# Performance work log

Measured on AMD Instinct MI355X. Metric: run time of the kernel, lower is better.

## Reference

```python
import jax, jax.numpy as jnp
import numpy as np

# ---- static geometry derived from truncation (matches torch __init__) ----
T = 127
N_LAT_NH = T + 1                                   # 128 NH latitudes
LONS = [20 + 4 * i for i in range(N_LAT_NH)]       # octahedral reduced grid
CUMS = np.concatenate([[0], np.cumsum(np.array(LONS + LONS[::-1]))]).astype(int)
HZW_NH = np.minimum(4 + np.arange(N_LAT_NH), T)    # cubic truncation: m_max = nlon//4 - 1, capped at T
N_LATS_PER_M = np.array([(HZW_NH >= m).sum() for m in range(T + 1)])
L_SYM_FULL = (T + 3) // 2                          # 65 rows before dropping row 0
L_ANT = (T + 2) // 2                               # 64
N_VARS = 128
BATCH, ENS = 4, 1


def _tri_masks():
    """Zero-padded triangular structure of the per-m Legendre matrices."""
    sym = np.zeros((T + 1, L_SYM_FULL, N_LAT_NH), np.float32)
    ant = np.zeros((T + 1, L_ANT, N_LAT_NH), np.float32)
    for m in range(T + 1):
        n_lats = int(N_LATS_PER_M[m])
        ms = (T - m + 3) // 2
        off = L_SYM_FULL - ms
        sym[m, off:, N_LAT_NH - n_lats:] = 1.0
        if (m + 1) % 2 == 1:
            sym[m, off, :] = 0.0
        ma = (T - m + 2) // 2
        off = L_ANT - ma
        ant[m, off:, N_LAT_NH - n_lats:] = 1.0
        if m % 2 == 1:
            ant[m, off, :] = 0.0
    return sym[:, 1:, :], ant   # module drops first symmetric row -> [128,64,128]


def setup_inputs() -> dict:
    key = jax.random.key(0)
    k1, k2, k3 = jax.random.split(key, 3)
    n_grid = int(CUMS[-1])
    x = jax.random.normal(k1, (BATCH, ENS, n_grid, N_VARS), jnp.float32)
    sm, am = _tri_masks()
    # random stand-ins for (gaussian-weight-fused) Legendre polynomials, with the exact
    # triangular zero structure the module builds from ecTrans assets
    symmetric = jax.random.normal(k2, sm.shape, jnp.float32) * jnp.asarray(sm)
    antisymmetric = jax.random.normal(k3, am.shape, jnp.float32) * jnp.asarray(am)
    return {"x": x, "symmetric": symmetric, "antisymmetric": antisymmetric}


def reference(x, symmetric, antisymmetric):
    """Octahedral SHT forward: ragged longitudinal rfft -> hemispheric fold -> per-m Legendre matmuls.

    Returns spectrum [b, e, l, m, vars, 2] (real/imag stacked on last axis).
    """
    n_lat = 2 * N_LAT_NH
    north, south = [], []
    # loop is over structurally distinct (ragged) latitude ring lengths; NH lat i and its
    # SH mirror (lat n_lat-1-i) share nlon/truncation, so batch them in one FFT call.
    for i in range(N_LAT_NH):
        j = n_lat - 1 - i
        nlon = LONS[i]
        xn = x[:, :, CUMS[i]:CUMS[i + 1], :]           # [b,e,nlon,v]
        xs = x[:, :, CUMS[j]:CUMS[j + 1], :]
        xp = jnp.stack([xn, xs], axis=2)               # [b,e,2,nlon,v]
        f = jnp.fft.rfft(xp, axis=3) / nlon            # torch norm='forward'
        m_hi = int(HZW_NH[i]) + 1                      # keep m <= highest zonal wavenumber
        f = f[:, :, :, :m_hi, :]
        f = jnp.pad(f, ((0, 0), (0, 0), (0, 0), (0, T + 1 - m_hi), (0, 0)))
        north.append(f[:, :, 0])
        south.append(f[:, :, 1])                       # index i <-> lat n_lat-1-i: already pole-mirrored
    north = jnp.stack(north, axis=2)                   # [b,e,n_lat_nh,m,v] complex64
    south = jnp.stack(south, axis=2)
    # hemispheric symmetry of Legendre polynomials
    sym = north + south
    anti = north - south
    # per-m truncated Legendre contractions over NH latitudes (n)
    out_s = jnp.einsum('mln,benmv->belmv', symmetric, sym)     # [b,e,64,m,v]
    out_a = jnp.einsum('mln,benmv->belmv', antisymmetric, anti)
    # interleave symmetric (l-m even) and antisymmetric (l-m odd) rows -> full l axis (128)
    spec = jnp.stack([out_s, out_a], axis=3)
    b, e, L, _, M, V = spec.shape
    spec = spec.reshape(b, e, 2 * L, M, V)             # [b,e,l,m,v] complex, lower triangle zeros
    return jnp.stack([spec.real, spec.imag], axis=-1)  # real view [b,e,l,m,v,2]
```

## Files before the change

kernel.cpp:

```cpp
#include <hip/hip_runtime.h>
#include <math.h>

#define NGRID 70144
#define NV 128
#define JT 16
#define VS 64

__device__ __forceinline__ float4 f4add(float4 a, float4 b){ return make_float4(a.x+b.x, a.y+b.y, a.z+b.z, a.w+b.w); }
__device__ __forceinline__ float4 f4sub(float4 a, float4 b){ return make_float4(a.x-b.x, a.y-b.y, a.z-b.z, a.w-b.w); }

__device__ __forceinline__ long twoff_of(int i){
  long off = 0;
  for(int k=0;k<i;k++){
    int mh = (5+k < 128) ? (5+k) : 128;
    off += (long)mh * (long)(11 + 2*k);
  }
  return off;
}

__global__ void fill_tw(float* __restrict__ tw){
  int ring = blockIdx.x, mc = blockIdx.y;
  int N = 20 + 4*ring, H = N/2;
  int mhi = (5+ring < 128) ? (5+ring) : 128;
  int m0 = mc*32;
  if(m0 >= mhi) return;
  int m1 = (m0+32 < mhi) ? (m0+32) : mhi;
  long base = twoff_of(ring);
  int tot = (m1-m0)*(H+1);
  float invN = 1.0f / (float)N;
  for(int idx = threadIdx.x; idx < tot; idx += blockDim.x){
    int m = m0 + idx/(H+1);
    int j = idx % (H+1);
    int p = (m*j) % N;
    float th = 6.2831853071795864f * (float)p * invN;
    float sn, cs;
    __sincosf(th, &sn, &cs);
    long o = (base + (long)(m)*(H+1) + j)*2;
    tw[o]   = cs * invN;
    tw[o+1] = -sn * invN;
  }
}

__global__ __launch_bounds__(256) void dft_fold(const float* __restrict__ x,
                                                const float* __restrict__ tw,
                                                float* __restrict__ G){
  int ring = 127 - blockIdx.x;
  int mt = blockIdx.y;
  int b  = blockIdx.z >> 1;
  int vh = blockIdx.z & 1;
  int N = 20 + 4*ring, H = N/2, JC = H+1;
  int mhi = (5+ring < 128) ? (5+ring) : 128;
  int mbase = mt*32;
  if(mbase >= mhi) return;

  __shared__ __align__(16) float cS[JT][VS], sS[JT][VS], cA[JT][VS], sA[JT][VS];
  __shared__ __align__(16) float twl[JT][32][2];

  int tid = threadIdx.x;
  int vl = tid & 63;
  int mg = tid >> 6;
  int v  = vh*64 + vl;

  long twbase = twoff_of(ring);
  long offN = (long)ring*(2*ring+18);
  long a = ring+1;
  long offS = (long)NGRID - a*(2*a+18);
  const float* xn = x + ((long)b*NGRID + offN)*NV + vh*64;
  const float* xs = x + ((long)b*NGRID + offS)*NV + vh*64;

  float aSR[8], aSI[8], aAR[8], aAI[8];
  #pragma unroll
  for(int k=0;k<8;k++){ aSR[k]=0.f; aSI[k]=0.f; aAR[k]=0.f; aAI[k]=0.f; }

  int sjj = tid >> 4;
  int sv4 = (tid & 15) << 2;
  int tmp2 = (tid & 15) << 1;

  for(int j0=0; j0<JC; j0+=JT){
    __syncthreads();
    {
      int j = j0 + sjj;
      float4 z = make_float4(0.f,0.f,0.f,0.f);
      float4 nj=z, sj=z, np=z, sp=z;
      if(j < JC){
        nj = *(const float4*)&xn[(long)j*NV + sv4];
        sj = *(const float4*)&xs[(long)j*NV + sv4];
        if(j > 0 && j < H){
          int jp = N - j;
          np = *(const float4*)&xn[(long)jp*NV + sv4];
          sp = *(const float4*)&xs[(long)jp*NV + sv4];
        }
      }
      float4 e  = f4add(nj, sj);
      float4 o  = f4sub(nj, sj);
      float4 ep = f4add(np, sp);
      float4 op = f4sub(np, sp);
      *(float4*)&cS[sjj][sv4] = f4add(e, ep);
      *(float4*)&sS[sjj][sv4] = f4sub(e, ep);
      *(float4*)&cA[sjj][sv4] = f4add(o, op);
      *(float4*)&sA[sjj][sv4] = f4sub(o, op);
    }
    {
      int jsrc = j0 + sjj; if(jsrc > H) jsrc = H;
      int m0s = mbase + tmp2;     if(m0s > mhi-1) m0s = mhi-1;
      int m1s = mbase + tmp2 + 1; if(m1s > mhi-1) m1s = mhi-1;
      float2 t0 = *(const float2*)&tw[(twbase + (long)m0s*JC + jsrc)*2];
      float2 t1 = *(const float2*)&tw[(twbase + (long)m1s*JC + jsrc)*2];
      *(float4*)&twl[sjj][tmp2][0] = make_float4(t0.x, t0.y, t1.x, t1.y);
    }
    __syncthreads();
    int jlim = JC - j0; if(jlim > JT) jlim = JT;
    for(int jj=0; jj<jlim; jj++){
      float c_s = cS[jj][vl], s_s = sS[jj][vl], c_a = cA[jj][vl], s_a = sA[jj][vl];
      const float* twrow = &twl[jj][mg*8][0];
      #pragma unroll
      for(int k2=0; k2<4; k2++){
        float4 t4 = *(const float4*)&twrow[k2*4];
        aSR[2*k2]   += c_s*t4.x;  aSI[2*k2]   += s_s*t4.y;
        aAR[2*k2]   += c_a*t4.x;  aAI[2*k2]   += s_a*t4.y;
        aSR[2*k2+1] += c_s*t4.z;  aSI[2*k2+1] += s_s*t4.w;
        aAR[2*k2+1] += c_a*t4.z;  aAI[2*k2+1] += s_a*t4.w;
      }
    }
  }
  long gb = (long)ring*1024 + (long)b*256 + (long)v*2;
  #pragma unroll
  for(int k=0;k<8;k++){
    int m = mbase + mg*8 + k;
    if(m < mhi){
      long o = (long)m*131072 + gb;
      *(float2*)&G[o]             = make_float2(aSR[k], aSI[k]);
      *(float2*)&G[o + 16777216L] = make_float2(aAR[k], aAI[k]);
    }
  }
}

__global__ __launch_bounds__(256) void legendre_mm(const float* __restrict__ Wsym,
                                                   const float* __restrict__ Want,
                                                   const float* __restrict__ G,
                                                   float* __restrict__ out){
  int m = blockIdx.x, b = blockIdx.y, s = blockIdx.z;
  const float* W = s ? Want : Wsym;
  __shared__ __align__(16) float Wt[128][68];
  int tid = threadIdx.x;
  const float* Wm = W + (long)m*8192;
  for(int idx=tid; idx<8192; idx+=256){
    int l = idx >> 7, n = idx & 127;
    Wt[n][l] = Wm[idx];
  }
  __syncthreads();
  int v = tid & 127, lh = tid >> 7;
  int n0 = (m-4 > 0) ? (m-4) : 0;
  const float* Gs = G + (long)s*16777216 + (long)m*131072 + (long)b*256 + (long)v*2;
  float aR[32], aI[32];
  #pragma unroll
  for(int q=0;q<32;q++){ aR[q]=0.f; aI[q]=0.f; }
  #pragma unroll 2
  for(int n=n0; n<128; n++){
    float2 g = *(const float2*)&Gs[(long)n*1024];
    const float* wrow = &Wt[n][lh*32];
    #pragma unroll
    for(int q2=0; q2<8; q2++){
      float4 w = *(const float4*)&wrow[q2*4];
      aR[q2*4+0] += w.x*g.x; aI[q2*4+0] += w.x*g.y;
      aR[q2*4+1] += w.y*g.x; aI[q2*4+1] += w.y*g.y;
      aR[q2*4+2] += w.z*g.x; aI[q2*4+2] += w.z*g.y;
      aR[q2*4+3] += w.w*g.x; aI[q2*4+3] += w.w*g.y;
    }
  }
  #pragma unroll
  for(int q=0;q<32;q++){
    int l = lh*32 + q;
    int lf = 2*l + s;
    long o = (((long)b*128 + lf)*128 + m)*256 + (long)v*2;
    *(float2*)&out[o] = make_float2(aR[q], aI[q]);
  }
}

extern "C" void kernel_launch(void* const* d_in, const int* in_sizes, int n_in,
                              void* d_out, int out_size, void* d_ws, size_t ws_size,
                              hipStream_t stream) {
  const float* x    = (const float*)d_in[0];
  const float* Wsym = (const float*)d_in[1];
  const float* Want = (const float*)d_in[2];
  float* out = (float*)d_out;
  float* ws  = (float*)d_ws;

  long two = 0;
  for(int k=0;k<128;k++){ int mh = (5+k<128)?(5+k):128; two += (long)mh*(long)(11+2*k); }
  long GBASE = (two*2 + 255) & ~255L;

  float* tw = ws;
  float* G  = ws + GBASE;

  hipLaunchKernelGGL(fill_tw,     dim3(128,4),   dim3(256), 0, stream, tw);
  hipLaunchKernelGGL(dft_fold,    dim3(128,4,8), dim3(256), 0, stream, x, tw, G);
  hipLaunchKernelGGL(legendre_mm, dim3(128,4,2), dim3(256), 0, stream, Wsym, Want, G, out);
}
```

Measured before the change: 428.8 us.

## Move Legendre contraction to bf16 MFMA with hi/lo split for precision

The FP32 FMA Legendre matmul is replaced by an MFMA kernel that uses bf16x3 emulation (hi*hi + lo*hi + hi*lo). The DFT stage now writes its output split into bf16 high and low parts. A new kernel splits the Legendre weights into bf16 hi/lo parts, reusing the twiddle workspace after the DFT stage has finished with it. The B tile is staged in swizzled shared memory, and all-zero K blocks are skipped for large m. This should cut ALU time in the matmul stage, at the cost of an extra launch and a small loss of accuracy from the dropped lo*lo term.

```diff
diff --git a/kernel.cpp b/kernel.cpp
--- a/kernel.cpp
+++ b/kernel.cpp
@@ -6,8 +6,17 @@
 #define JT 16
 #define VS 64
 
+typedef float f32x4 __attribute__((ext_vector_type(4)));
+typedef short short8 __attribute__((ext_vector_type(8)));
+
 __device__ __forceinline__ float4 f4add(float4 a, float4 b){ return make_float4(a.x+b.x, a.y+b.y, a.z+b.z, a.w+b.w); }
 __device__ __forceinline__ float4 f4sub(float4 a, float4 b){ return make_float4(a.x-b.x, a.y-b.y, a.z-b.z, a.w-b.w); }
+
+__device__ __forceinline__ unsigned f2bf(float f){
+  unsigned u = __float_as_uint(f);
+  return (u + 0x7FFFu + ((u>>16)&1u)) >> 16;
+}
+__device__ __forceinline__ float bf2f(unsigned h){ return __uint_as_float(h<<16); }
 
 __device__ __forceinline__ long twoff_of(int i){
   long off = 0;
@@ -43,7 +52,8 @@
 
 __global__ __launch_bounds__(256) void dft_fold(const float* __restrict__ x,
                                                 const float* __restrict__ tw,
-                                                float* __restrict__ G){
+                                                unsigned short* __restrict__ Gh,
+                                                unsigned short* __restrict__ Gl){
   int ring = 127 - blockIdx.x;
   int mt = blockIdx.y;
   int b  = blockIdx.z >> 1;
@@ -129,51 +139,102 @@
     int m = mbase + mg*8 + k;
     if(m < mhi){
       long o = (long)m*131072 + gb;
-      *(float2*)&G[o]             = make_float2(aSR[k], aSI[k]);
-      *(float2*)&G[o + 16777216L] = make_float2(aAR[k], aAI[k]);
-    }
-  }
-}
-
-__global__ __launch_bounds__(256) void legendre_mm(const float* __restrict__ Wsym,
-                                                   const float* __restrict__ Want,
-                                                   const float* __restrict__ G,
-                                                   float* __restrict__ out){
+      unsigned h0 = f2bf(aSR[k]), h1 = f2bf(aSI[k]);
+      unsigned l0 = f2bf(aSR[k] - bf2f(h0)), l1 = f2bf(aSI[k] - bf2f(h1));
+      *(unsigned*)&Gh[o] = h0 | (h1<<16);
+      *(unsigned*)&Gl[o] = l0 | (l1<<16);
+      unsigned a0 = f2bf(aAR[k]), a1 = f2bf(aAI[k]);
+      unsigned b0 = f2bf(aAR[k] - bf2f(a0)), b1 = f2bf(aAI[k] - bf2f(a1));
+      *(unsigned*)&Gh[o + 16777216L] = a0 | (a1<<16);
+      *(unsigned*)&Gl[o + 16777216L] = b0 | (b1<<16);
+    }
+  }
+}
+
+__global__ void w_split(const float* __restrict__ Wsym, const float* __restrict__ Want,
+                        unsigned short* __restrict__ Wh, unsigned short* __restrict__ Wl){
+  long i = (long)blockIdx.x*256 + threadIdx.x;
+  const float* W = (i < 1048576) ? Wsym : Want;
+  float w = W[i & 1048575];
+  unsigned h = f2bf(w);
+  unsigned l = f2bf(w - bf2f(h));
+  Wh[i] = (unsigned short)h;
+  Wl[i] = (unsigned short)l;
+}
+
+__global__ __launch_bounds__(256) void legendre_mfma(const unsigned short* __restrict__ Wh,
+                                                     const unsigned short* __restrict__ Wl,
+                                                     const unsigned short* __restrict__ Gh,
+                                                     const unsigned short* __restrict__ Gl,
+                                                     float* __restrict__ out){
   int m = blockIdx.x, b = blockIdx.y, s = blockIdx.z;
-  const float* W = s ? Want : Wsym;
-  __shared__ __align__(16) float Wt[128][68];
+  __shared__ __align__(16) unsigned short Bhs[8192];
+  __shared__ __align__(16) unsigned short Bls[8192];
   int tid = threadIdx.x;
-  const float* Wm = W + (long)m*8192;
-  for(int idx=tid; idx<8192; idx+=256){
-    int l = idx >> 7, n = idx & 127;
-    Wt[n][l] = Wm[idx];
-  }
-  __syncthreads();
-  int v = tid & 127, lh = tid >> 7;
-  int n0 = (m-4 > 0) ? (m-4) : 0;
-  const float* Gs = G + (long)s*16777216 + (long)m*131072 + (long)b*256 + (long)v*2;
-  float aR[32], aI[32];
-  #pragma unroll
-  for(int q=0;q<32;q++){ aR[q]=0.f; aI[q]=0.f; }
-  #pragma unroll 2
-  for(int n=n0; n<128; n++){
-    float2 g = *(const float2*)&Gs[(long)n*1024];
-    const float* wrow = &Wt[n][lh*32];
-    #pragma unroll
-    for(int q2=0; q2<8; q2++){
-      float4 w = *(const float4*)&wrow[q2*4];
-      aR[q2*4+0] += w.x*g.x; aI[q2*4+0] += w.x*g.y;
-      aR[q2*4+1] += w.y*g.x; aI[q2*4+1] += w.y*g.y;
-      aR[q2*4+2] += w.z*g.x; aI[q2*4+2] += w.z*g.y;
-      aR[q2*4+3] += w.w*g.x; aI[q2*4+3] += w.w*g.y;
-    }
-  }
-  #pragma unroll
-  for(int q=0;q<32;q++){
-    int l = lh*32 + q;
-    int lf = 2*l + s;
-    long o = (((long)b*128 + lf)*128 + m)*256 + (long)v*2;
-    *(float2*)&out[o] = make_float2(aR[q], aI[q]);
+  int wave = tid >> 6, lane = tid & 63;
+  int j = lane & 15, kb = lane >> 4;
+
+  int kt0 = (m > 4) ? ((m-4) >> 5) : 0;
+
+  const unsigned short* WA = Wh + (long)(s*128+m)*8192;
+  const unsigned short* WB = Wl + (long)(s*128+m)*8192;
+  long gBase = (long)(s*128+m)*131072 + (long)b*256 + tid;
+
+  f32x4 acc[4][4];
+  #pragma unroll
+  for(int a=0;a<4;a++)
+    #pragma unroll
+    for(int q=0;q<4;q++) acc[a][q] = (f32x4){0.f,0.f,0.f,0.f};
+
+  for(int kt=kt0; kt<4; ++kt){
+    #pragma unroll
+    for(int o=0;o<4;o++){
+      long nb = gBase + (long)(kt*32 + o*8)*1024;
+      unsigned p0=Gh[nb], p1=Gh[nb+1024], p2=Gh[nb+2048], p3=Gh[nb+3072],
+               p4=Gh[nb+4096], p5=Gh[nb+5120], p6=Gh[nb+6144], p7=Gh[nb+7168];
+      int4 pk = make_int4((int)(p0|(p1<<16)), (int)(p2|(p3<<16)),
+                          (int)(p4|(p5<<16)), (int)(p6|(p7<<16)));
+      *(int4*)&Bhs[tid*32 + ((o ^ (tid&3))<<3)] = pk;
+      unsigned q0=Gl[nb], q1=Gl[nb+1024], q2=Gl[nb+2048], q3=Gl[nb+3072],
+               q4=Gl[nb+4096], q5=Gl[nb+5120], q6=Gl[nb+6144], q7=Gl[nb+7168];
+      int4 qk = make_int4((int)(q0|(q1<<16)), (int)(q2|(q3<<16)),
+                          (int)(q4|(q5<<16)), (int)(q6|(q7<<16)));
+      *(int4*)&Bls[tid*32 + ((o ^ (tid&3))<<3)] = qk;
+    }
+    __syncthreads();
+    short8 ah[4], al[4];
+    #pragma unroll
+    for(int Mt=0;Mt<4;Mt++){
+      const unsigned short* ap = WA + (Mt*16 + j)*128 + kt*32 + kb*8;
+      ah[Mt] = *(const short8*)ap;
+      al[Mt] = *(const short8*)(WB + (Mt*16 + j)*128 + kt*32 + kb*8);
+    }
+    #pragma unroll
+    for(int nt=0;nt<4;nt++){
+      int c = (wave*4+nt)*16 + j;
+      short8 bh = *(short8*)&Bhs[c*32 + ((kb ^ (c&3))<<3)];
+      short8 bl = *(short8*)&Bls[c*32 + ((kb ^ (c&3))<<3)];
+      #pragma unroll
+      for(int Mt=0;Mt<4;Mt++){
+        acc[Mt][nt] = __builtin_amdgcn_mfma_f32_16x16x32_bf16(ah[Mt], bh, acc[Mt][nt], 0, 0, 0);
+        acc[Mt][nt] = __builtin_amdgcn_mfma_f32_16x16x32_bf16(al[Mt], bh, acc[Mt][nt], 0, 0, 0);
+        acc[Mt][nt] = __builtin_amdgcn_mfma_f32_16x16x32_bf16(ah[Mt], bl, acc[Mt][nt], 0, 0, 0);
+      }
+    }
+    __syncthreads();
+  }
+  int r4 = (lane>>4)<<2;
+  #pragma unroll
+  for(int Mt=0;Mt<4;Mt++){
+    #pragma unroll
+    for(int nt=0;nt<4;nt++){
+      int c = (wave*4+nt)*16 + j;
+      #pragma unroll
+      for(int reg=0;reg<4;reg++){
+        int l = Mt*16 + r4 + reg;
+        out[((long)(b*128 + 2*l + s)*128 + m)*256 + c] = acc[Mt][nt][reg];
+      }
+    }
   }
 }
 
@@ -191,9 +252,13 @@
   long GBASE = (two*2 + 255) & ~255L;
 
   float* tw = ws;
-  float* G  = ws + GBASE;
-
-  hipLaunchKernelGGL(fill_tw,     dim3(128,4),   dim3(256), 0, stream, tw);
-  hipLaunchKernelGGL(dft_fold,    dim3(128,4,8), dim3(256), 0, stream, x, tw, G);
-  hipLaunchKernelGGL(legendre_mm, dim3(128,4,2), dim3(256), 0, stream, Wsym, Want, G, out);
-}
+  unsigned short* Wh = (unsigned short*)ws;
+  unsigned short* Wl = Wh + 2097152;
+  unsigned short* Gh = (unsigned short*)(ws + GBASE);
+  unsigned short* Gl = Gh + 33554432L;
+
+  hipLaunchKernelGGL(fill_tw,       dim3(128,4),   dim3(256), 0, stream, tw);
+  hipLaunchKernelGGL(dft_fold,      dim3(128,4,8), dim3(256), 0, stream, x, tw, Gh, Gl);
+  hipLaunchKernelGGL(w_split,       dim3(8192),    dim3(256), 0, stream, Wsym, Want, Wh, Wl);
+  hipLaunchKernelGGL(legendre_mfma, dim3(128,4,2), dim3(256), 0, stream, Wh, Wl, Gh, Gl, out);
+}
```

Result: faster. 417.1 us (-2.7%).
